# Kernel optimization log

Hardware: AMD Instinct MI355X
Metric: run time of the kernel (lower is better)

Reference implementation:

```python
import jax, jax.numpy as jnp
import numpy as np
from jax.scipy.special import logsumexp

T_MIN, T_MAX = 0.1, 1.0
NEG_INF = -jnp.inf


def setup_inputs() -> dict:
    key = jax.random.key(0)
    k1, k2 = jax.random.split(key)
    B, I, J, D = 4, 64, 512, 256
    return {
        "text_embeddings": jax.random.normal(k1, (B, I, D), jnp.float32),
        "mel_embeddings": jax.random.normal(k2, (B, J, D), jnp.float32),
        "text_mask": jnp.ones((B, I), dtype=bool),
        "mel_mask": jnp.ones((B, J), dtype=bool),
        "temperature_ratio": jnp.asarray(1.0, jnp.float32),
    }


def _moboligner_forward(text_embeddings, mel_embeddings, text_mask, mel_mask, temperature_ratio):
    B, I, D_t = text_embeddings.shape
    J, D_m = mel_embeddings.shape[1], mel_embeddings.shape[2]

    # energy (B, I, J)
    energy = jnp.einsum("bid,bjd->bij", text_embeddings, mel_embeddings) / np.sqrt(D_t * D_m)

    # Gumbel noise + temperature (deterministic key stands in for torch.rand_like)
    temp = T_MIN + (T_MAX - T_MIN) * temperature_ratio
    u = jax.random.uniform(jax.random.key(42), energy.shape, energy.dtype, 1e-20, 1.0)
    energy = (energy - jnp.log(-jnp.log(u))) / temp

    # ---- masks over the 4D (B, I, J, K=J) tensor (alpha direction, K = J) ----
    jj = jnp.arange(J)
    ii = jnp.arange(I)
    Ilen = text_mask.sum(1)  # (B,)
    tri = jj[:, None] > jj[None, :]  # (J, K): boundary i+1 strictly after boundary i
    # feasible frame range for boundary row i:  i+1 <= j <= J - Ilen + i + 1
    lo = ii[:, None] + 1                                   # (I, 1)
    hi = J - Ilen[:, None, None] + ii[None, :, None] + 1   # (B, I, 1)
    range_ok = (jj[None, None, :] >= lo[None]) & (jj[None, None, :] <= hi)  # (B, I, J)

    # energy_4D with masked fills (soft -1000 for out-of-range, -inf for structurally invalid)
    e4 = jnp.broadcast_to(energy[..., None], (B, I, J, J))
    soft_ok = range_ok & mel_mask[:, None, :] & text_mask[:, :, None]      # (B, I, J)
    e4 = jnp.where(soft_ok[..., None], e4, -1000.0)
    hard_ok = tri[None, None] & mel_mask[:, None, None, :]                 # (B,1,J,K)-ish
    e4 = jnp.where(hard_ok, e4, NEG_INF)

    # normalize over j -> log P(B_{i+1} = j | B_i = k)
    lse_j = logsumexp(e4, axis=2, keepdims=True)
    lcp = e4 - jnp.where(jnp.isfinite(lse_j), lse_j, 0.0)  # (B, I, J, K)

    # log P(B_{i+1} >= j | B_i = k): reverse logcumsumexp over j
    lcp_geq = jnp.flip(jax.lax.cumlogsumexp(jnp.flip(lcp, axis=2), axis=2), axis=2)
    lcp_geq = jnp.where(tri[None, None], lcp_geq, NEG_INF)

    # ---- alpha DP: alpha[b,i,c] = LSE_k( alpha[b,i-1,k] + lcp[b,i-1,c-1,k] ) ----
    alpha0 = jnp.full((B, J + 1), NEG_INF).at[:, 0].set(0.0)
    lcp_rows = jnp.moveaxis(lcp, 1, 0)  # (I, B, J, K)

    def step(prev, xs):
        lcp_i, i = xs  # lcp_i: (B, J, K), prev: (B, J+1) cols 0..J
        vals = logsumexp(prev[:, None, :-1] + lcp_i, axis=-1)  # (B, J) -> cols 1..J
        row = jnp.concatenate([jnp.full((prev.shape[0], 1), NEG_INF), vals], axis=1)
        row = jnp.where(jnp.arange(row.shape[1])[None, :] >= i, row, NEG_INF)
        return row, row

    _, rows = jax.lax.scan(step, alpha0, (lcp_rows[: I - 1], jnp.arange(1, I)))
    alpha = jnp.concatenate([alpha0[:, None], jnp.moveaxis(rows, 0, 1)], axis=1)  # (B, I, J+1)

    # ---- delta: delta[b,i,j] = LSE_k( alpha[b,i,k] + lcp_geq[b,i,j,k] ) with k<j ----
    a = alpha[:, :, :-1]                      # (B, I, K)
    t = jnp.swapaxes(lcp_geq, 2, 3)           # (B, I, K, J)
    ul = jj[:, None] < jj[None, :]            # (K, J) valid where k < j
    x = jnp.where(ul[None, None], a[..., None] + t, -10.0)
    delta = logsumexp(x, axis=2)              # (B, I, J) log soft alignment

    w = jnp.exp(delta)
    expanded = jnp.einsum("bij,bid->bjd", w, text_embeddings)  # (B, J, D_text)
    return delta, expanded


def reference(text_embeddings, mel_embeddings, text_mask, mel_mask, temperature_ratio):
    return _moboligner_forward(text_embeddings, mel_embeddings, text_mask, mel_mask, temperature_ratio)
```

## Files before the change

kernel.cpp:

```cpp
#include <hip/hip_runtime.h>
#include <hip/hip_bf16.h>
#include <math.h>


#define B_ 4
#define I_ 64
#define J_ 512
#define D_ 256

#define NEGINF (-INFINITY)
#define LOG2E 1.4426950408889634f
#define CUTF (-720.0f)
#define MIDCLAMP 60.0f
#define FLOORK 4.5399929762484854e-05f

__device__ __forceinline__ void tf2x32(unsigned int x0, unsigned int x1,
                                       unsigned int& y0, unsigned int& y1) {
  const unsigned int k0 = 0u, k1 = 42u;
  const unsigned int k2 = k0 ^ k1 ^ 0x1BD11BDAu;
  x0 += k0; x1 += k1;
#define TFR(r) { x0 += x1; x1 = (x1 << r) | (x1 >> (32 - r)); x1 ^= x0; }
  TFR(13) TFR(15) TFR(26) TFR(6)   x0 += k1; x1 += k2 + 1u;
  TFR(17) TFR(29) TFR(16) TFR(24)  x0 += k2; x1 += k0 + 2u;
  TFR(13) TFR(15) TFR(26) TFR(6)   x0 += k0; x1 += k1 + 3u;
  TFR(17) TFR(29) TFR(16) TFR(24)  x0 += k1; x1 += k2 + 4u;
  TFR(13) TFR(15) TFR(26) TFR(6)   x0 += k2; x1 += k0 + 5u;
#undef TFR
  y0 = x0; y1 = x1;
}

__device__ __forceinline__ unsigned int rand_bits(unsigned int n) {
  unsigned int y0, y1;
  tf2x32(0u, n, y0, y1);
  return y0 ^ y1;
}

__device__ __forceinline__ float gumbel_term(unsigned int n) {
  unsigned int bits = rand_bits(n);
  float f = __uint_as_float((bits >> 9) | 0x3f800000u) - 1.0f;
  float u = fmaxf(f + 1e-20f, 1e-20f);
  return logf(-logf(u));
}

struct MS { float m; float s; };

__device__ __forceinline__ MS ms_comb(MS a, MS b) {
  if (b.m == NEGINF) return a;
  if (a.m == NEGINF) return b;
  MS r;
  if (a.m >= b.m) { r.m = a.m; r.s = a.s + b.s * __expf(b.m - a.m); }
  else            { r.m = b.m; r.s = b.s + a.s * __expf(a.m - b.m); }
  return r;
}
__device__ __forceinline__ MS ms_add(MS a, float x) {
  if (x == NEGINF) return a;
  if (a.m == NEGINF) { MS r; r.m = x; r.s = 1.0f; return r; }
  MS r;
  if (a.m >= x) { r.m = a.m; r.s = a.s + __expf(x - a.m); }
  else          { r.m = x;   r.s = 1.0f + a.s * __expf(a.m - x); }
  return r;
}
__device__ __forceinline__ float ms_val(MS a) {
  if (a.m == NEGINF) return NEGINF;
  return a.m + __logf(a.s);
}

__device__ __forceinline__ MS wave_incl_scan(MS v, int lane) {
  #pragma unroll
  for (int off = 1; off < 64; off <<= 1) {
    float mo = __shfl_up(v.m, off, 64);
    float so = __shfl_up(v.s, off, 64);
    if (lane >= off) { MS o; o.m = mo; o.s = so; v = ms_comb(o, v); }
  }
  return v;
}

template<int CTRL, int RM, int BM, bool BC>
__device__ __forceinline__ float dppf(float oldv, float src) {
  return __int_as_float(__builtin_amdgcn_update_dpp(
      __float_as_int(oldv), __float_as_int(src), CTRL, RM, BM, BC));
}

__device__ __forceinline__ float wave_incl_add_f(float x) {
  x += dppf<0x111, 0xf, 0xf, false>(0.0f, x);
  x += dppf<0x112, 0xf, 0xf, false>(0.0f, x);
  x += dppf<0x114, 0xf, 0xf, false>(0.0f, x);
  x += dppf<0x118, 0xf, 0xf, false>(0.0f, x);
  x += dppf<0x142, 0xa, 0xf, false>(0.0f, x);
  x += dppf<0x143, 0xc, 0xf, false>(0.0f, x);
  return x;
}

__device__ __forceinline__ bool mask_is_byte(const unsigned char* p) {
  const unsigned int* w = (const unsigned int*)p;
  unsigned int orbits = 0;
  #pragma unroll
  for (int k = 0; k < 16; k++) orbits |= w[k];
  return (orbits & 0xFFFFFF00u) != 0u;
}
__device__ __forceinline__ int mask_get(const unsigned char* p, int idx, bool isbyte) {
  return isbyte ? (p[idx] != 0) : (((const int*)p)[idx] != 0);
}

__global__ __launch_bounds__(512) void kernelA(
    const float* __restrict__ text, const float* __restrict__ mel,
    const unsigned char* __restrict__ tmask, const unsigned char* __restrict__ mmask,
    const float* __restrict__ tratio,
    float* __restrict__ val2, float* __restrict__ sgeq2) {
  int bi = blockIdx.x;
  int b = bi >> 6, i = bi & 63;
  int tid = threadIdx.x;

  __shared__ float t_s[D_];
  __shared__ float v_s[J_];
  __shared__ int sh_ilen;

  const bool tbyte = mask_is_byte(tmask);
  const bool mbyte = mask_is_byte(mmask);
  const int tok = mask_get(tmask, b * I_ + i, tbyte);

  if (tid < 64) {
    int mk = mask_get(tmask, b * I_ + tid, tbyte);
    unsigned long long bal = __ballot(mk != 0);
    if (tid == 0) sh_ilen = (int)__popcll(bal);
  }
  if (tid < D_) t_s[tid] = text[(size_t)(b * I_ + i) * D_ + tid];
  __syncthreads();

  int j = tid;
  const float4* m4 = (const float4*)(mel + (size_t)(b * J_ + j) * D_);
  const float4* t4 = (const float4*)t_s;
  float4 acc; acc.x = acc.y = acc.z = acc.w = 0.0f;
  #pragma unroll 8
  for (int d4 = 0; d4 < D_ / 4; ++d4) {
    float4 a = m4[d4]; float4 t = t4[d4];
    acc.x += a.x * t.x; acc.y += a.y * t.y;
    acc.z += a.z * t.z; acc.w += a.w * t.w;
  }
  float dot = (acc.x + acc.y) + (acc.z + acc.w);

  float temp = 0.1f + 0.9f * tratio[0];
  float gum = gumbel_term((unsigned)((b * I_ + i) * J_ + j));
  float e = (dot * (1.0f / 256.0f) - gum) / temp;
  int mok = mask_get(mmask, b * J_ + j, mbyte);
  int hi = J_ - sh_ilen + i + 1;
  bool ok = (j >= i + 1) && (j <= hi) && mok && tok;
  float v = ok ? e : -1000.0f;
  v_s[j] = v;
  val2[(size_t)bi * J_ + j] = v * LOG2E;
  __syncthreads();

  if (tid < 64) {
    int l = tid;
    float xs[8];
    MS tot; tot.m = NEGINF; tot.s = 0.0f;
    #pragma unroll
    for (int e = 0; e < 8; e++) {
      int p = l * 8 + e;
      xs[e] = v_s[J_ - 1 - p];
      tot = ms_add(tot, xs[e]);
    }
    MS inc = wave_incl_scan(tot, l);
    MS ex; ex.m = __shfl_up(inc.m, 1, 64); ex.s = __shfl_up(inc.s, 1, 64);
    if (l == 0) { ex.m = NEGINF; ex.s = 0.0f; }
    MS run = ex;
    #pragma unroll
    for (int e = 0; e < 8; e++) {
      int p = l * 8 + e;
      run = ms_add(run, xs[e]);
      sgeq2[(size_t)bi * J_ + (J_ - 1 - p)] = ms_val(run) * LOG2E;
    }
  }
}

__global__ __launch_bounds__(64) void kernelB(
    const float* __restrict__ val2, const float* __restrict__ sgeq2,
    const unsigned char* __restrict__ mmask, const float* __restrict__ tratio,
    float* __restrict__ aw, float* __restrict__ sw) {
  const int b = blockIdx.x;
  const int l = threadIdx.x;
  const int p0 = l << 3;

  const float temp = 0.1f + 0.9f * tratio[0];
  const float Tfix = 1442.695f / temp + 40.0f;

  const bool mbyte = mask_is_byte(mmask);
  float ilimf[8], Atm[8], Asel[8];
#pragma unroll
  for (int e = 0; e < 8; e++) {
    int p = p0 + e;
    bool ok = (p <= J_ - 2) && (mask_get(mmask, b * J_ + p, mbyte) != 0);
    ilimf[e] = ok ? (float)(p - 1) : -1.5f;
    Atm[e] = 0.0f;
    Asel[e] = (p == 0) ? 1.0f : 0.0f;
  }

  const float4* sb4 = (const float4*)(sgeq2 + (size_t)b * I_ * J_);
  const float4* vb4 = (const float4*)(val2  + (size_t)b * I_ * J_);
  float* ab = aw + (size_t)b * I_ * J_;
  float* wb = sw + (size_t)b * I_ * J_;

  float4 Sq0 = sb4[l * 2], Sq1 = sb4[l * 2 + 1];
  float4 Vq0 = vb4[l * 2], Vq1 = vb4[l * 2 + 1];

  for (int i = 0; i < I_; i++) {
    const int rn = (i + 1 < I_) ? i + 1 : i;
    const int ro = rn * (J_ / 4);
    float4 Sn0 = sb4[ro + l * 2], Sn1 = sb4[ro + l * 2 + 1];
    float4 Vn0 = vb4[ro + l * 2], Vn1 = vb4[ro + l * 2 + 1];

    float S[8] = {Sq0.x, Sq0.y, Sq0.z, Sq0.w, Sq1.x, Sq1.y, Sq1.z, Sq1.w};
    float V[8] = {Vq0.x, Vq0.y, Vq0.z, Vq0.w, Vq1.x, Vq1.y, Vq1.z, Vq1.w};

    float nextS0 = dppf<0x130, 0xf, 0xf, false>(0.0f, S[0]);
    float sp1s[8];
    bool spk[8];
#pragma unroll
    for (int e = 0; e < 8; e++) {
      float sp1 = (e < 7) ? S[e + 1] : nextS0;
      spk[e] = sp1 < CUTF;
      sp1s[e] = spk[e] ? (sp1 + Tfix) : sp1;
    }

    float h[8], t[8];
#pragma unroll
    for (int e = 0; e < 8; e++) {
      float arg = fminf(Atm[e] - sp1s[e], MIDCLAMP);
      float x = __builtin_amdgcn_exp2f(arg) * Asel[e];
      h[e] = spk[e] ? 0.0f : x;
      t[e] = spk[e] ? x : 0.0f;
    }

    float hp[8], tp[8];
    hp[0] = h[0]; tp[0] = t[0];
#pragma unroll
    for (int e = 1; e < 8; e++) { hp[e] = hp[e - 1] + h[e]; tp[e] = tp[e - 1] + t[e]; }

    float hincl = wave_incl_add_f(hp[7]);
    float tincl = wave_incl_add_f(tp[7]);
    float hx = dppf<0x138, 0xf, 0xf, false>(0.0f, hincl);
    float tx = dppf<0x138, 0xf, 0xf, false>(0.0f, tincl);

    float sel[8], Ts[8], ao[8];
#pragma unroll
    for (int e = 0; e < 8; e++) {
      float pe1 = (e >= 1) ? hx + hp[e - 1] : hx;
      float tv1 = (e >= 1) ? tx + tp[e - 1] : tx;
      bool tl = tv1 > 0.0f;
      sel[e] = tl ? tv1 : pe1;
      Ts[e]  = tl ? Tfix : 0.0f;
      ao[e]  = S[e] + Ts[e];
    }
    float4* a4 = (float4*)(ab + (size_t)i * J_);
    a4[l * 2]     = make_float4(ao[0], ao[1], ao[2], ao[3]);
    a4[l * 2 + 1] = make_float4(ao[4], ao[5], ao[6], ao[7]);
    float4* s4 = (float4*)(wb + (size_t)i * J_);
    s4[l * 2]     = make_float4(sel[0], sel[1], sel[2], sel[3]);
    s4[l * 2 + 1] = make_float4(sel[4], sel[5], sel[6], sel[7]);

    if (i < I_ - 1) {
      float prevV7 = dppf<0x138, 0xf, 0xf, false>(0.0f, V[7]);
      float prevT7 = dppf<0x138, 0xf, 0xf, false>(0.0f, Ts[7]);
      float prevS7 = dppf<0x138, 0xf, 0xf, false>(0.0f, sel[7]);
      float fi = (float)i;
#pragma unroll
      for (int e = 0; e < 8; e++) {
        float vp = (e >= 1) ? V[e - 1]   : prevV7;
        float ts = (e >= 1) ? Ts[e - 1]  : prevT7;
        float sl = (e >= 1) ? sel[e - 1] : prevS7;
        Atm[e] = vp + ts;
        Asel[e] = (fi <= ilimf[e]) ? sl : 0.0f;
      }
    }
    Sq0 = Sn0; Sq1 = Sn1; Vq0 = Vn0; Vq1 = Vn1;
  }
}

__global__ __launch_bounds__(256) void kernelCD(
    const float* __restrict__ aw, const float* __restrict__ sw,
    const float* __restrict__ text,
    float* __restrict__ expanded, float* __restrict__ delta) {
  int blk = blockIdx.x;
  if (blk < B_ * J_) {
    int b = blk >> 9, j = blk & (J_ - 1);
    int d = threadIdx.x;
    __shared__ float w_s[I_];
    float fl = (float)(J_ - j) * FLOORK;
    if (d < I_) {
      size_t idx = (size_t)(b * I_ + d) * J_ + j;
      w_s[d] = fmaf(__builtin_amdgcn_exp2f(aw[idx]), sw[idx], fl);
    }
    __syncthreads();
    float acc = 0.0f;
    #pragma unroll 8
    for (int i = 0; i < I_; i++)
      acc += w_s[i] * text[(size_t)(b * I_ + i) * D_ + d];
    expanded[(size_t)(b * J_ + j) * D_ + d] = acc;
  } else {
    int n = (blk - B_ * J_) * 256 + threadIdx.x;
    int q = n & (J_ - 1);
    float fl = (float)(J_ - q) * FLOORK;
    float w = fmaf(__builtin_amdgcn_exp2f(aw[n]), sw[n], fl);
    delta[n] = __logf(w);
  }
}

extern "C" void kernel_launch(void* const* d_in, const int* in_sizes, int n_in,
                              void* d_out, int out_size, void* d_ws, size_t ws_size,
                              hipStream_t stream) {
  (void)in_sizes; (void)n_in; (void)out_size; (void)ws_size;
  const float* text = (const float*)d_in[0];
  const float* mel  = (const float*)d_in[1];
  const unsigned char* tmask = (const unsigned char*)d_in[2];
  const unsigned char* mmask = (const unsigned char*)d_in[3];
  const float* tratio = (const float*)d_in[4];

  float* out = (float*)d_out;
  float* delta = out;
  float* expanded = out + (size_t)B_ * I_ * J_;
  float* val2  = (float*)d_ws;
  float* sgeq2 = val2 + (size_t)B_ * I_ * J_;
  float* aw    = sgeq2 + (size_t)B_ * I_ * J_;
  float* sw    = aw + (size_t)B_ * I_ * J_;

  kernelA<<<B_ * I_, 512, 0, stream>>>(text, mel, tmask, mmask, tratio, val2, sgeq2);
  kernelB<<<B_, 64, 0, stream>>>(val2, sgeq2, mmask, tratio, aw, sw);
  kernelCD<<<B_ * J_ + (B_ * I_ * J_) / 256, 256, 0, stream>>>(
      aw, sw, text, expanded, delta);
}
```

Before: 67.76 us.

## Fuse three kernels into one cooperative kernel with grid-wide syncs

Merges the energy/scan kernel, the sequential alpha recurrence, and the expansion/delta kernel into a single cooperative launch of 256 blocks of 512 threads, separated by grid.sync(). The aim is to remove the launch gaps between the three kernels. In exchange, the final stage runs on far fewer threads than the old separate kernel, which launched one block per (b,j) row plus extra blocks for delta. Each block now processes two rows at a time in a loop with extra __syncthreads(). Grid syncs also add their own overhead, and most blocks sit idle during the serial phase that only 4 blocks execute.

```diff
diff --git a/kernel.cpp b/kernel.cpp
--- a/kernel.cpp
+++ b/kernel.cpp
@@ -1,6 +1,9 @@
 #include <hip/hip_runtime.h>
 #include <hip/hip_bf16.h>
+#include <hip/hip_cooperative_groups.h>
 #include <math.h>
+
+namespace cg = cooperative_groups;
 
 
 #define B_ 4
@@ -102,202 +105,207 @@
   return isbyte ? (p[idx] != 0) : (((const int*)p)[idx] != 0);
 }
 
-__global__ __launch_bounds__(512) void kernelA(
+__global__ __launch_bounds__(512) void fusedK(
     const float* __restrict__ text, const float* __restrict__ mel,
     const unsigned char* __restrict__ tmask, const unsigned char* __restrict__ mmask,
     const float* __restrict__ tratio,
-    float* __restrict__ val2, float* __restrict__ sgeq2) {
-  int bi = blockIdx.x;
-  int b = bi >> 6, i = bi & 63;
-  int tid = threadIdx.x;
+    float* __restrict__ val2, float* __restrict__ sgeq2,
+    float* __restrict__ aw, float* __restrict__ sw,
+    float* __restrict__ expanded, float* __restrict__ delta) {
+  cg::grid_group grid = cg::this_grid();
+  const int blk = blockIdx.x;
+  const int tid = threadIdx.x;
 
   __shared__ float t_s[D_];
   __shared__ float v_s[J_];
   __shared__ int sh_ilen;
-
-  const bool tbyte = mask_is_byte(tmask);
-  const bool mbyte = mask_is_byte(mmask);
-  const int tok = mask_get(tmask, b * I_ + i, tbyte);
-
-  if (tid < 64) {
-    int mk = mask_get(tmask, b * I_ + tid, tbyte);
-    unsigned long long bal = __ballot(mk != 0);
-    if (tid == 0) sh_ilen = (int)__popcll(bal);
-  }
-  if (tid < D_) t_s[tid] = text[(size_t)(b * I_ + i) * D_ + tid];
-  __syncthreads();
-
-  int j = tid;
-  const float4* m4 = (const float4*)(mel + (size_t)(b * J_ + j) * D_);
-  const float4* t4 = (const float4*)t_s;
-  float4 acc; acc.x = acc.y = acc.z = acc.w = 0.0f;
-  #pragma unroll 8
-  for (int d4 = 0; d4 < D_ / 4; ++d4) {
-    float4 a = m4[d4]; float4 t = t4[d4];
-    acc.x += a.x * t.x; acc.y += a.y * t.y;
-    acc.z += a.z * t.z; acc.w += a.w * t.w;
-  }
-  float dot = (acc.x + acc.y) + (acc.z + acc.w);
-
-  float temp = 0.1f + 0.9f * tratio[0];
-  float gum = gumbel_term((unsigned)((b * I_ + i) * J_ + j));
-  float e = (dot * (1.0f / 256.0f) - gum) / temp;
-  int mok = mask_get(mmask, b * J_ + j, mbyte);
-  int hi = J_ - sh_ilen + i + 1;
-  bool ok = (j >= i + 1) && (j <= hi) && mok && tok;
-  float v = ok ? e : -1000.0f;
-  v_s[j] = v;
-  val2[(size_t)bi * J_ + j] = v * LOG2E;
-  __syncthreads();
-
-  if (tid < 64) {
-    int l = tid;
-    float xs[8];
-    MS tot; tot.m = NEGINF; tot.s = 0.0f;
-    #pragma unroll
+  __shared__ float w_s[2][I_];
+
+  {
+    const int b = blk >> 6, i = blk & 63;
+    const bool tbyte = mask_is_byte(tmask);
+    const bool mbyte = mask_is_byte(mmask);
+    const int tok = mask_get(tmask, b * I_ + i, tbyte);
+
+    if (tid < 64) {
+      int mk = mask_get(tmask, b * I_ + tid, tbyte);
+      unsigned long long bal = __ballot(mk != 0);
+      if (tid == 0) sh_ilen = (int)__popcll(bal);
+    }
+    if (tid < D_) t_s[tid] = text[(size_t)(b * I_ + i) * D_ + tid];
+    __syncthreads();
+
+    int j = tid;
+    const float4* m4 = (const float4*)(mel + (size_t)(b * J_ + j) * D_);
+    const float4* t4 = (const float4*)t_s;
+    float4 acc; acc.x = acc.y = acc.z = acc.w = 0.0f;
+    #pragma unroll 8
+    for (int d4 = 0; d4 < D_ / 4; ++d4) {
+      float4 a = m4[d4]; float4 t = t4[d4];
+      acc.x += a.x * t.x; acc.y += a.y * t.y;
+      acc.z += a.z * t.z; acc.w += a.w * t.w;
+    }
+    float dot = (acc.x + acc.y) + (acc.z + acc.w);
+
+    float temp = 0.1f + 0.9f * tratio[0];
+    float gum = gumbel_term((unsigned)((b * I_ + i) * J_ + j));
+    float e = (dot * (1.0f / 256.0f) - gum) / temp;
+    int mok = mask_get(mmask, b * J_ + j, mbyte);
+    int hi = J_ - sh_ilen + i + 1;
+    bool ok = (j >= i + 1) && (j <= hi) && mok && tok;
+    float v = ok ? e : -1000.0f;
+    v_s[j] = v;
+    val2[(size_t)blk * J_ + j] = v * LOG2E;
+    __syncthreads();
+
+    if (tid < 64) {
+      int l = tid;
+      float xs[8];
+      MS tot; tot.m = NEGINF; tot.s = 0.0f;
+      #pragma unroll
+      for (int e2 = 0; e2 < 8; e2++) {
+        int p = l * 8 + e2;
+        xs[e2] = v_s[J_ - 1 - p];
+        tot = ms_add(tot, xs[e2]);
+      }
+      MS inc = wave_incl_scan(tot, l);
+      MS ex; ex.m = __shfl_up(inc.m, 1, 64); ex.s = __shfl_up(inc.s, 1, 64);
+      if (l == 0) { ex.m = NEGINF; ex.s = 0.0f; }
+      MS run = ex;
+      #pragma unroll
+      for (int e2 = 0; e2 < 8; e2++) {
+        int p = l * 8 + e2;
+        run = ms_add(run, xs[e2]);
+        sgeq2[(size_t)blk * J_ + (J_ - 1 - p)] = ms_val(run) * LOG2E;
+      }
+    }
+  }
+
+  grid.sync();
+
+  if (blk < B_ && tid < 64) {
+    const int b = blk;
+    const int l = tid;
+    const int p0 = l << 3;
+
+    const float temp = 0.1f + 0.9f * tratio[0];
+    const float Tfix = 1442.695f / temp + 40.0f;
+
+    const bool mbyte = mask_is_byte(mmask);
+    float ilimf[8], Atm[8], Asel[8];
+#pragma unroll
     for (int e = 0; e < 8; e++) {
-      int p = l * 8 + e;
-      xs[e] = v_s[J_ - 1 - p];
-      tot = ms_add(tot, xs[e]);
-    }
-    MS inc = wave_incl_scan(tot, l);
-    MS ex; ex.m = __shfl_up(inc.m, 1, 64); ex.s = __shfl_up(inc.s, 1, 64);
-    if (l == 0) { ex.m = NEGINF; ex.s = 0.0f; }
-    MS run = ex;
-    #pragma unroll
-    for (int e = 0; e < 8; e++) {
-      int p = l * 8 + e;
-      run = ms_add(run, xs[e]);
-      sgeq2[(size_t)bi * J_ + (J_ - 1 - p)] = ms_val(run) * LOG2E;
-    }
-  }
-}
-
-__global__ __launch_bounds__(64) void kernelB(
-    const float* __restrict__ val2, const float* __restrict__ sgeq2,
-    const unsigned char* __restrict__ mmask, const float* __restrict__ tratio,
-    float* __restrict__ aw, float* __restrict__ sw) {
-  const int b = blockIdx.x;
-  const int l = threadIdx.x;
-  const int p0 = l << 3;
-
-  const float temp = 0.1f + 0.9f * tratio[0];
-  const float Tfix = 1442.695f / temp + 40.0f;
-
-  const bool mbyte = mask_is_byte(mmask);
-  float ilimf[8], Atm[8], Asel[8];
-#pragma unroll
-  for (int e = 0; e < 8; e++) {
-    int p = p0 + e;
-    bool ok = (p <= J_ - 2) && (mask_get(mmask, b * J_ + p, mbyte) != 0);
-    ilimf[e] = ok ? (float)(p - 1) : -1.5f;
-    Atm[e] = 0.0f;
-    Asel[e] = (p == 0) ? 1.0f : 0.0f;
-  }
-
-  const float4* sb4 = (const float4*)(sgeq2 + (size_t)b * I_ * J_);
-  const float4* vb4 = (const float4*)(val2  + (size_t)b * I_ * J_);
-  float* ab = aw + (size_t)b * I_ * J_;
-  float* wb = sw + (size_t)b * I_ * J_;
-
-  float4 Sq0 = sb4[l * 2], Sq1 = sb4[l * 2 + 1];
-  float4 Vq0 = vb4[l * 2], Vq1 = vb4[l * 2 + 1];
-
-  for (int i = 0; i < I_; i++) {
-    const int rn = (i + 1 < I_) ? i + 1 : i;
-    const int ro = rn * (J_ / 4);
-    float4 Sn0 = sb4[ro + l * 2], Sn1 = sb4[ro + l * 2 + 1];
-    float4 Vn0 = vb4[ro + l * 2], Vn1 = vb4[ro + l * 2 + 1];
-
-    float S[8] = {Sq0.x, Sq0.y, Sq0.z, Sq0.w, Sq1.x, Sq1.y, Sq1.z, Sq1.w};
-    float V[8] = {Vq0.x, Vq0.y, Vq0.z, Vq0.w, Vq1.x, Vq1.y, Vq1.z, Vq1.w};
-
-    float nextS0 = dppf<0x130, 0xf, 0xf, false>(0.0f, S[0]);
-    float sp1s[8];
-    bool spk[8];
-#pragma unroll
-    for (int e = 0; e < 8; e++) {
-      float sp1 = (e < 7) ? S[e + 1] : nextS0;
-      spk[e] = sp1 < CUTF;
-      sp1s[e] = spk[e] ? (sp1 + Tfix) : sp1;
-    }
-
-    float h[8], t[8];
-#pragma unroll
-    for (int e = 0; e < 8; e++) {
-      float arg = fminf(Atm[e] - sp1s[e], MIDCLAMP);
-      float x = __builtin_amdgcn_exp2f(arg) * Asel[e];
-      h[e] = spk[e] ? 0.0f : x;
-      t[e] = spk[e] ? x : 0.0f;
-    }
-
-    float hp[8], tp[8];
-    hp[0] = h[0]; tp[0] = t[0];
-#pragma unroll
-    for (int e = 1; e < 8; e++) { hp[e] = hp[e - 1] + h[e]; tp[e] = tp[e - 1] + t[e]; }
-
-    float hincl = wave_incl_add_f(hp[7]);
-    float tincl = wave_incl_add_f(tp[7]);
-    float hx = dppf<0x138, 0xf, 0xf, false>(0.0f, hincl);
-    float tx = dppf<0x138, 0xf, 0xf, false>(0.0f, tincl);
-
-    float sel[8], Ts[8], ao[8];
-#pragma unroll
-    for (int e = 0; e < 8; e++) {
-      float pe1 = (e >= 1) ? hx + hp[e - 1] : hx;
-      float tv1 = (e >= 1) ? tx + tp[e - 1] : tx;
-      bool tl = tv1 > 0.0f;
-      sel[e] = tl ? tv1 : pe1;
-      Ts[e]  = tl ? Tfix : 0.0f;
-      ao[e]  = S[e] + Ts[e];
-    }
-    float4* a4 = (float4*)(ab + (size_t)i * J_);
-    a4[l * 2]     = make_float4(ao[0], ao[1], ao[2], ao[3]);
-    a4[l * 2 + 1] = make_float4(ao[4], ao[5], ao[6], ao[7]);
-    float4* s4 = (float4*)(wb + (size_t)i * J_);
-    s4[l * 2]     = make_float4(sel[0], sel[1], sel[2], sel[3]);
-    s4[l * 2 + 1] = make_float4(sel[4], sel[5], sel[6], sel[7]);
-
-    if (i < I_ - 1) {
-      float prevV7 = dppf<0x138, 0xf, 0xf, false>(0.0f, V[7]);
-      float prevT7 = dppf<0x138, 0xf, 0xf, false>(0.0f, Ts[7]);
-      float prevS7 = dppf<0x138, 0xf, 0xf, false>(0.0f, sel[7]);
-      float fi = (float)i;
+      int p = p0 + e;
+      bool ok = (p <= J_ - 2) && (mask_get(mmask, b * J_ + p, mbyte) != 0);
+      ilimf[e] = ok ? (float)(p - 1) : -1.5f;
+      Atm[e] = 0.0f;
+      Asel[e] = (p == 0) ? 1.0f : 0.0f;
+    }
+
+    const float4* sb4 = (const float4*)(sgeq2 + (size_t)b * I_ * J_);
+    const float4* vb4 = (const float4*)(val2  + (size_t)b * I_ * J_);
+    float* ab = aw + (size_t)b * I_ * J_;
+    float* wb = sw + (size_t)b * I_ * J_;
+
+    float4 Sq0 = sb4[l * 2], Sq1 = sb4[l * 2 + 1];
+    float4 Vq0 = vb4[l * 2], Vq1 = vb4[l * 2 + 1];
+
+    for (int i = 0; i < I_; i++) {
+      const int rn = (i + 1 < I_) ? i + 1 : i;
+      const int ro = rn * (J_ / 4);
+      float4 Sn0 = sb4[ro + l * 2], Sn1 = sb4[ro + l * 2 + 1];
+      float4 Vn0 = vb4[ro + l * 2], Vn1 = vb4[ro + l * 2 + 1];
+
+      float S[8] = {Sq0.x, Sq0.y, Sq0.z, Sq0.w, Sq1.x, Sq1.y, Sq1.z, Sq1.w};
+      float V[8] = {Vq0.x, Vq0.y, Vq0.z, Vq0.w, Vq1.x, Vq1.y, Vq1.z, Vq1.w};
+
+      float nextS0 = dppf<0x130, 0xf, 0xf, false>(0.0f, S[0]);
+      float sp1s[8];
+      bool spk[8];
 #pragma unroll
       for (int e = 0; e < 8; e++) {
-        float vp = (e >= 1) ? V[e - 1]   : prevV7;
-        float ts = (e >= 1) ? Ts[e - 1]  : prevT7;
-        float sl = (e >= 1) ? sel[e - 1] : prevS7;
-        Atm[e] = vp + ts;
-        Asel[e] = (fi <= ilimf[e]) ? sl : 0.0f;
-      }
-    }
-    Sq0 = Sn0; Sq1 = Sn1; Vq0 = Vn0; Vq1 = Vn1;
-  }
-}
-
-__global__ __launch_bounds__(256) void kernelCD(
-    const float* __restrict__ aw, const float* __restrict__ sw,
-    const float* __restrict__ text,
-    float* __restrict__ expanded, float* __restrict__ delta) {
-  int blk = blockIdx.x;
-  if (blk < B_ * J_) {
-    int b = blk >> 9, j = blk & (J_ - 1);
-    int d = threadIdx.x;
-    __shared__ float w_s[I_];
-    float fl = (float)(J_ - j) * FLOORK;
-    if (d < I_) {
-      size_t idx = (size_t)(b * I_ + d) * J_ + j;
-      w_s[d] = fmaf(__builtin_amdgcn_exp2f(aw[idx]), sw[idx], fl);
-    }
-    __syncthreads();
-    float acc = 0.0f;
-    #pragma unroll 8
-    for (int i = 0; i < I_; i++)
-      acc += w_s[i] * text[(size_t)(b * I_ + i) * D_ + d];
-    expanded[(size_t)(b * J_ + j) * D_ + d] = acc;
-  } else {
-    int n = (blk - B_ * J_) * 256 + threadIdx.x;
+        float sp1 = (e < 7) ? S[e + 1] : nextS0;
+        spk[e] = sp1 < CUTF;
+        sp1s[e] = spk[e] ? (sp1 + Tfix) : sp1;
+      }
+
+      float h[8], t[8];
+#pragma unroll
+      for (int e = 0; e < 8; e++) {
+        float arg = fminf(Atm[e] - sp1s[e], MIDCLAMP);
+        float x = __builtin_amdgcn_exp2f(arg) * Asel[e];
+        h[e] = spk[e] ? 0.0f : x;
+        t[e] = spk[e] ? x : 0.0f;
+      }
+
+      float hp[8], tp[8];
+      hp[0] = h[0]; tp[0] = t[0];
+#pragma unroll
+      for (int e = 1; e < 8; e++) { hp[e] = hp[e - 1] + h[e]; tp[e] = tp[e - 1] + t[e]; }
+
+      float hincl = wave_incl_add_f(hp[7]);
+      float tincl = wave_incl_add_f(tp[7]);
+      float hx = dppf<0x138, 0xf, 0xf, false>(0.0f, hincl);
+      float tx = dppf<0x138, 0xf, 0xf, false>(0.0f, tincl);
+
+      float sel[8], Ts[8], ao[8];
+#pragma unroll
+      for (int e = 0; e < 8; e++) {
+        float pe1 = (e >= 1) ? hx + hp[e - 1] : hx;
+        float tv1 = (e >= 1) ? tx + tp[e - 1] : tx;
+        bool tl = tv1 > 0.0f;
+        sel[e] = tl ? tv1 : pe1;
+        Ts[e]  = tl ? Tfix : 0.0f;
+        ao[e]  = S[e] + Ts[e];
+      }
+      float4* a4 = (float4*)(ab + (size_t)i * J_);
+      a4[l * 2]     = make_float4(ao[0], ao[1], ao[2], ao[3]);
+      a4[l * 2 + 1] = make_float4(ao[4], ao[5], ao[6], ao[7]);
+      float4* s4 = (float4*)(wb + (size_t)i * J_);
+      s4[l * 2]     = make_float4(sel[0], sel[1], sel[2], sel[3]);
+      s4[l * 2 + 1] = make_float4(sel[4], sel[5], sel[6], sel[7]);
+
+      if (i < I_ - 1) {
+        float prevV7 = dppf<0x138, 0xf, 0xf, false>(0.0f, V[7]);
+        float prevT7 = dppf<0x138, 0xf, 0xf, false>(0.0f, Ts[7]);
+        float prevS7 = dppf<0x138, 0xf, 0xf, false>(0.0f, sel[7]);
+        float fi = (float)i;
+#pragma unroll
+        for (int e = 0; e < 8; e++) {
+          float vp = (e >= 1) ? V[e - 1]   : prevV7;
+          float ts = (e >= 1) ? Ts[e - 1]  : prevT7;
+          float sl = (e >= 1) ? sel[e - 1] : prevS7;
+          Atm[e] = vp + ts;
+          Asel[e] = (fi <= ilimf[e]) ? sl : 0.0f;
+        }
+      }
+      Sq0 = Sn0; Sq1 = Sn1; Vq0 = Vn0; Vq1 = Vn1;
+    }
+  }
+
+  grid.sync();
+
+  {
+    const int half = tid >> 8;
+    const int d = tid & 255;
+    for (int t = blk * 2 + half; t < B_ * J_; t += 2 * 256) {
+      int b = t >> 9, j = t & (J_ - 1);
+      float fl = (float)(J_ - j) * FLOORK;
+      if (d < I_) {
+        size_t idx = (size_t)(b * I_ + d) * J_ + j;
+        w_s[half][d] = fmaf(__builtin_amdgcn_exp2f(aw[idx]), sw[idx], fl);
+      }
+      __syncthreads();
+      float acc = 0.0f;
+      #pragma unroll 8
+      for (int i = 0; i < I_; i++)
+        acc += w_s[half][i] * text[(size_t)(b * I_ + i) * D_ + d];
+      expanded[(size_t)(b * J_ + j) * D_ + d] = acc;
+      __syncthreads();
+    }
+  }
+  {
+    int n = blk * 512 + tid;
     int q = n & (J_ - 1);
     float fl = (float)(J_ - q) * FLOORK;
     float w = fmaf(__builtin_amdgcn_exp2f(aw[n]), sw[n], fl);
@@ -323,8 +331,11 @@
   float* aw    = sgeq2 + (size_t)B_ * I_ * J_;
   float* sw    = aw + (size_t)B_ * I_ * J_;
 
-  kernelA<<<B_ * I_, 512, 0, stream>>>(text, mel, tmask, mmask, tratio, val2, sgeq2);
-  kernelB<<<B_, 64, 0, stream>>>(val2, sgeq2, mmask, tratio, aw, sw);
-  kernelCD<<<B_ * J_ + (B_ * I_ * J_) / 256, 256, 0, stream>>>(
-      aw, sw, text, expanded, delta);
-}
+  void* args[] = {
+    (void*)&text, (void*)&mel, (void*)&tmask, (void*)&mmask, (void*)&tratio,
+    (void*)&val2, (void*)&sgeq2, (void*)&aw, (void*)&sw,
+    (void*)&expanded, (void*)&delta
+  };
+  hipLaunchCooperativeKernel((const void*)fusedK, dim3(B_ * I_), dim3(512),
+                             args, 0, stream);
+}
```

After: 131.7 us. 1.94x slower.
